# Kernel tuning notes

Hardware: AMD Instinct MI355X
Metric: run time of the kernel (lower is better)

The kernel has to match this reference:

```python
import jax, jax.numpy as jnp
import numpy as np

DIM = 1024
HEADS = 16
HD = DIM // HEADS
EPS = 1e-5


def setup_inputs() -> dict:
    key = jax.random.key(0)
    ks = jax.random.split(key, 7)
    s = 0.02
    return {
        "x": jax.random.normal(ks[0], (2, 2048, DIM), dtype=jnp.float32),
        "w_qkv": jax.random.normal(ks[1], (DIM, 3 * DIM), dtype=jnp.float32) * s,
        "b_qkv": jnp.zeros((3 * DIM,), dtype=jnp.float32),
        "g_q": jnp.ones((HD,), dtype=jnp.float32),
        "be_q": jnp.zeros((HD,), dtype=jnp.float32),
        "g_k": jnp.ones((HD,), dtype=jnp.float32),
        "be_k": jnp.zeros((HD,), dtype=jnp.float32),
        "w_proj": jax.random.normal(ks[2], (DIM, DIM), dtype=jnp.float32) * s,
        "b_proj": jnp.zeros((DIM,), dtype=jnp.float32),
    }


def _ln(x, g, b):
    mu = jnp.mean(x, axis=-1, keepdims=True)
    var = jnp.var(x, axis=-1, keepdims=True)
    return (x - mu) * jax.lax.rsqrt(var + EPS) * g + b


def reference(x, w_qkv, b_qkv, g_q, be_q, g_k, be_k, w_proj, b_proj):
    B, N, C = x.shape
    qkv = x @ w_qkv + b_qkv                      # [B,N,3C]
    qkv = qkv.reshape(B, N, 3, HEADS, HD).transpose(2, 0, 3, 1, 4)  # [3,B,H,N,hd]
    q, k, v = qkv[0], qkv[1], qkv[2]
    q = _ln(q, g_q, be_q) * (HD ** -0.5)
    k = _ln(k, g_k, be_k)
    attn = jax.nn.softmax(jnp.einsum("bhqd,bhkd->bhqk", q, k), axis=-1)
    out = jnp.einsum("bhqk,bhkd->bhqd", attn, v)  # [B,H,N,hd]
    out = out.transpose(0, 2, 1, 3).reshape(B, N, C)
    return out @ w_proj + b_proj
```

## Files before the change

### kernel.cpp

```cpp
#include <hip/hip_runtime.h>
#include <hip/hip_bf16.h>


typedef short bf16x8 __attribute__((ext_vector_type(8)));
typedef float f32x4  __attribute__((ext_vector_type(4)));

__device__ __forceinline__ short f2bf(float f) {
  union { float f; unsigned u; } c; c.f = f;
  unsigned r = c.u + 0x7fffu + ((c.u >> 16) & 1u);
  return (short)(r >> 16);
}

__device__ __forceinline__ unsigned pk2(float a, float b) {
  __hip_bfloat162 h = __float22bfloat162_rn(make_float2(a, b));
  unsigned u;
  __builtin_memcpy(&u, &h, 4);
  return u;
}

__device__ __forceinline__ void gld16(const void* g, void* l) {
  __builtin_amdgcn_global_load_lds(
      (const __attribute__((address_space(1))) unsigned int*)(unsigned long long)g,
      (__attribute__((address_space(3))) unsigned int*)(unsigned int)(unsigned long long)l,
      16, 0, 0);
}

__global__ void k_cvt(const float* __restrict__ in, short* __restrict__ out, int n) {
  int i = (blockIdx.x * blockDim.x + threadIdx.x) * 4;
  if (i < n) {
    float4 f = *(const float4*)(in + i);
    uint2 u;
    u.x = pk2(f.x, f.y);
    u.y = pk2(f.z, f.w);
    *(uint2*)(out + i) = u;
  }
}

__global__ void k_transpose(const float* __restrict__ in, short* __restrict__ out,
                            int R, int C) {
  __shared__ float t[32][33];
  const int tx = threadIdx.x, ty = threadIdx.y;
  const int c0 = blockIdx.x * 32, r0 = blockIdx.y * 32;
#pragma unroll
  for (int i = 0; i < 4; i++)
    t[ty * 4 + i][tx] = in[(size_t)(r0 + ty * 4 + i) * C + c0 + tx];
  __syncthreads();
#pragma unroll
  for (int i = 0; i < 4; i++)
    out[(size_t)(c0 + ty * 4 + i) * R + r0 + tx] = f2bf(t[tx][ty * 4 + i]);
}

__device__ __forceinline__ void mm_loop(const short* __restrict__ A,
                                        const short* __restrict__ B,
                                        int K, int mBase, int nBase,
                                        short* As, short* Bs, f32x4 acc[4][4]) {
  const int tid = threadIdx.x;
  const int w = tid >> 6, lane = tid & 63;
  const int wr = w >> 1, wc = w & 1;
  const int lhi = lane >> 4, llo = lane & 15;
  const int rin = lane >> 3;
  const int kin = (lane & 7) * 8;

  const f32x4 fz = {0.f, 0.f, 0.f, 0.f};
#pragma unroll
  for (int mi = 0; mi < 4; mi++)
#pragma unroll
    for (int ni = 0; ni < 4; ni++) acc[mi][ni] = fz;

  const int nkt = K >> 6;

  const short* pA[4];
  const short* pB[4];
#pragma unroll
  for (int i = 0; i < 4; i++) {
    const int row = (w * 4 + i) * 8 + rin;
    pA[i] = A + (size_t)(mBase + row) * K + kin;
    pB[i] = B + (size_t)(nBase + row) * K + kin;
  }

#define MMSTAGE(buf)                                                           \
  {                                                                            \
    _Pragma("unroll")                                                          \
    for (int i = 0; i < 4; i++) {                                              \
      const int c = w * 4 + i;                                                 \
      gld16(pA[i], As + (buf) * 8192 + c * 512);                               \
      gld16(pB[i], Bs + (buf) * 8192 + c * 512);                               \
      pA[i] += 64;                                                             \
      pB[i] += 64;                                                             \
    }                                                                          \
  }

  MMSTAGE(0);
  __syncthreads();
  int cur = 0;

  for (int kb = 0; kb < nkt; kb++) {
    if (kb + 1 < nkt) MMSTAGE(cur ^ 1);
    const short* Ac = As + cur * 8192;
    const short* Bc = Bs + cur * 8192;
#pragma unroll
    for (int kk = 0; kk < 2; kk++) {
      bf16x8 a[4], b[4];
#pragma unroll
      for (int mi = 0; mi < 4; mi++)
        a[mi] = *(const bf16x8*)(Ac + (wr * 64 + mi * 16 + llo) * 64 + kk * 32 + lhi * 8);
#pragma unroll
      for (int ni = 0; ni < 4; ni++)
        b[ni] = *(const bf16x8*)(Bc + (wc * 64 + ni * 16 + llo) * 64 + kk * 32 + lhi * 8);
#pragma unroll
      for (int mi = 0; mi < 4; mi++)
#pragma unroll
        for (int ni = 0; ni < 4; ni++)
          acc[mi][ni] = __builtin_amdgcn_mfma_f32_16x16x32_bf16(a[mi], b[ni], acc[mi][ni], 0, 0, 0);
    }
    __syncthreads();
    cur ^= 1;
  }
#undef MMSTAGE
}

__global__ __launch_bounds__(256) void k_gemm_qkv(
    const short* __restrict__ A, const short* __restrict__ B,
    const float* __restrict__ bqkv,
    const float* __restrict__ g_q, const float* __restrict__ be_q,
    const float* __restrict__ g_k, const float* __restrict__ be_k,
    short* __restrict__ Qg, short* __restrict__ Kg, short* __restrict__ Vtg) {
  __shared__ short As[2 * 8192];
  __shared__ short Bs[2 * 8192];
  f32x4 acc[4][4];
  const int mBase = blockIdx.x * 128, nBase = blockIdx.y * 128;
  mm_loop(A, B, 1024, mBase, nBase, As, Bs, acc);

  const int tid = threadIdx.x;
  const int w = tid >> 6, lane = tid & 63;
  const int wr = w >> 1, wc = w & 1;
  const int lhi = lane >> 4, llo = lane & 15;

  const int cg0 = nBase + wc * 64;
  const int t = cg0 >> 10;
  const int h = (cg0 & 1023) >> 6;

  float bias[4], gg[4], bb[4];
#pragma unroll
  for (int ni = 0; ni < 4; ni++) {
    const int d = ni * 16 + llo;
    bias[ni] = bqkv[cg0 + d];
    if (t == 0)      { gg[ni] = g_q[d]; bb[ni] = be_q[d]; }
    else if (t == 1) { gg[ni] = g_k[d]; bb[ni] = be_k[d]; }
    else             { gg[ni] = 1.f;    bb[ni] = 0.f; }
  }

#pragma unroll
  for (int mi = 0; mi < 4; mi++) {
    float v[4][4];
#pragma unroll
    for (int ni = 0; ni < 4; ni++)
#pragma unroll
      for (int j = 0; j < 4; j++) v[ni][j] = acc[mi][ni][j] + bias[ni];

    if (t < 2) {
#pragma unroll
      for (int j = 0; j < 4; j++) {
        float s = 0.f, s2 = 0.f;
#pragma unroll
        for (int ni = 0; ni < 4; ni++) { s += v[ni][j]; s2 += v[ni][j] * v[ni][j]; }
#pragma unroll
        for (int msk = 1; msk < 16; msk <<= 1) {
          s  += __shfl_xor(s,  msk, 64);
          s2 += __shfl_xor(s2, msk, 64);
        }
        const float mu = s * 0.015625f;
        const float var = s2 * 0.015625f - mu * mu;
        const float rs = rsqrtf(var + 1e-5f);
#pragma unroll
        for (int ni = 0; ni < 4; ni++) {
          float y = (v[ni][j] - mu) * rs * gg[ni] + bb[ni];
          if (t == 0) y *= 0.125f;
          v[ni][j] = y;
        }
      }
    }
    const int rbase = mBase + wr * 64 + mi * 16 + lhi * 4;
#pragma unroll
    for (int j = 0; j < 4; j++) {
      const int r = rbase + j;
      const int b_ = r >> 11;
      const int n = r & 2047;
      const int bh = b_ * 16 + h;
#pragma unroll
      for (int np = 0; np < 2; np++) {
        const int d0 = np * 32 + llo;
        const unsigned u = pk2(v[np * 2][j], v[np * 2 + 1][j]);
        const short lo = (short)(u & 0xffffu);
        const short hi = (short)(u >> 16);
        if (t == 0) {
          Qg[((size_t)bh * 2048 + n) * 64 + d0]      = lo;
          Qg[((size_t)bh * 2048 + n) * 64 + d0 + 16] = hi;
        } else if (t == 1) {
          Kg[((size_t)bh * 2048 + n) * 64 + d0]      = lo;
          Kg[((size_t)bh * 2048 + n) * 64 + d0 + 16] = hi;
        } else {
          Vtg[((size_t)bh * 64 + d0) * 2048 + n]        = lo;
          Vtg[((size_t)bh * 64 + d0 + 16) * 2048 + n]   = hi;
        }
      }
    }
  }
}

__global__ __launch_bounds__(256) void k_attn(const short* __restrict__ Qg,
                                              const short* __restrict__ Kg,
                                              const short* __restrict__ Vtg,
                                              short* __restrict__ aout) {
  __shared__ short KV[2][8192];
  __shared__ short Ps[4][1024];
  const int tid = threadIdx.x;
  const int w = tid >> 6, lane = tid & 63;
  const int lhi = lane >> 4, llo = lane & 15;
  const int rin = lane >> 3;
  const int tg = (lane & 7) ^ rin;
  const int bh = blockIdx.y;
  const int qrow0 = blockIdx.x * 64 + w * 16;

  const short* Qrow = Qg + ((size_t)bh * 2048 + qrow0 + llo) * 64;
  const bf16x8 qa0 = *(const bf16x8*)(Qrow + lhi * 8);
  const bf16x8 qa1 = *(const bf16x8*)(Qrow + 32 + lhi * 8);

  bf16x8 onesb;
#pragma unroll
  for (int e = 0; e < 8; e++) onesb[e] = (short)0x3F80;

  const f32x4 fz = {0.f, 0.f, 0.f, 0.f};
  f32x4 o[4];
#pragma unroll
  for (int dg = 0; dg < 4; dg++) o[dg] = fz;
  f32x4 lsum = fz;

  short* Pw = Ps[w];
  const size_t kbase = (size_t)bh * 2048;
  const size_t vbase = (size_t)bh * 64;

  const short* gp[4];
#pragma unroll
  for (int i = 0; i < 4; i++) {
    const int cc = w * 4 + i;
    gp[i] = (cc < 8)
        ? (Kg  + (kbase + (size_t)(cc * 8 + rin)) * 64 + tg * 8)
        : (Vtg + (vbase + (size_t)((cc - 8) * 8 + rin)) * 2048 + tg * 8);
  }
  const int gstride = (w < 2) ? 4096 : 64;

#define STAGE(buf)                                                             \
  {                                                                            \
    _Pragma("unroll")                                                          \
    for (int i = 0; i < 4; i++) {                                              \
      gld16(gp[i], &KV[buf][(w * 4 + i) * 512]);                               \
      gp[i] += gstride;                                                        \
    }                                                                          \
  }

  STAGE(0);
  __syncthreads();
  int cur = 0;

  for (int kt = 0; kt < 32; kt++) {
    if (kt < 31) STAGE(cur ^ 1);

    const short* Kc = KV[cur];
    const short* Vc = KV[cur] + 4096;

    f32x4 s[4];
    __builtin_amdgcn_s_setprio(1);
#pragma unroll
    for (int krg = 0; krg < 4; krg++) {
      const int rk = krg * 16 + llo;
      const int sw = rk & 7;
      const bf16x8 kb0 = *(const bf16x8*)(Kc + rk * 64 + ((lhi ^ sw)) * 8);
      const bf16x8 kb1 = *(const bf16x8*)(Kc + rk * 64 + (((4 + lhi) ^ sw)) * 8);
      f32x4 z = fz;
      z = __builtin_amdgcn_mfma_f32_16x16x32_bf16(kb0, qa0, z, 0, 0, 0);
      z = __builtin_amdgcn_mfma_f32_16x16x32_bf16(kb1, qa1, z, 0, 0, 0);
      s[krg] = z;
    }
    __builtin_amdgcn_s_setprio(0);

#pragma unroll
    for (int krg = 0; krg < 4; krg++) {
      const float p0 = __expf(s[krg][0]);
      const float p1 = __expf(s[krg][1]);
      const float p2 = __expf(s[krg][2]);
      const float p3 = __expf(s[krg][3]);
      uint2 u;
      u.x = pk2(p0, p1);
      u.y = pk2(p2, p3);
      char* pb = (char*)Pw + llo * 128 +
                 (((krg * 2 + (lhi >> 1)) ^ (llo & 7)) << 4) + ((lhi & 1) << 3);
      *(uint2*)pb = u;
    }

    const int swp = llo & 7;
    const bf16x8 pa0 = *(const bf16x8*)(Pw + llo * 64 + ((lhi ^ swp)) * 8);
    const bf16x8 pa1 = *(const bf16x8*)(Pw + llo * 64 + (((4 + lhi) ^ swp)) * 8);

    __builtin_amdgcn_s_setprio(1);
    lsum = __builtin_amdgcn_mfma_f32_16x16x32_bf16(pa0, onesb, lsum, 0, 0, 0);
    lsum = __builtin_amdgcn_mfma_f32_16x16x32_bf16(pa1, onesb, lsum, 0, 0, 0);

#pragma unroll
    for (int dg = 0; dg < 4; dg++) {
      const int rv = dg * 16 + llo;
      const int swv = rv & 7;
      const bf16x8 vb0 = *(const bf16x8*)(Vc + rv * 64 + ((lhi ^ swv)) * 8);
      const bf16x8 vb1 = *(const bf16x8*)(Vc + rv * 64 + (((4 + lhi) ^ swv)) * 8);
      o[dg] = __builtin_amdgcn_mfma_f32_16x16x32_bf16(pa0, vb0, o[dg], 0, 0, 0);
      o[dg] = __builtin_amdgcn_mfma_f32_16x16x32_bf16(pa1, vb1, o[dg], 0, 0, 0);
    }
    __builtin_amdgcn_s_setprio(0);
    __syncthreads();
    cur ^= 1;
  }
#undef STAGE

  const int b_ = bh >> 4, h = bh & 15;
#pragma unroll
  for (int j = 0; j < 4; j++) {
    const float inv = 1.f / lsum[j];
    const int n = qrow0 + lhi * 4 + j;
    short* arow = aout + ((size_t)(b_ * 2048 + n)) * 1024 + h * 64 + llo;
#pragma unroll
    for (int dp = 0; dp < 2; dp++) {
      const unsigned u = pk2(o[dp * 2][j] * inv, o[dp * 2 + 1][j] * inv);
      arow[dp * 32]      = (short)(u & 0xffffu);
      arow[dp * 32 + 16] = (short)(u >> 16);
    }
  }
}

__global__ __launch_bounds__(256) void k_gemm_proj(const short* __restrict__ A,
                                                   const short* __restrict__ B,
                                                   const float* __restrict__ bias,
                                                   float* __restrict__ C) {
  __shared__ short As[2 * 8192];
  __shared__ short Bs[2 * 8192];
  f32x4 acc[4][4];
  const int mBase = blockIdx.x * 128, nBase = blockIdx.y * 128;
  mm_loop(A, B, 1024, mBase, nBase, As, Bs, acc);

  const int tid = threadIdx.x;
  const int w = tid >> 6, lane = tid & 63;
  const int wr = w >> 1, wc = w & 1;
  const int lhi = lane >> 4, llo = lane & 15;
#pragma unroll
  for (int mi = 0; mi < 4; mi++)
#pragma unroll
    for (int ni = 0; ni < 4; ni++) {
      const int col = nBase + wc * 64 + ni * 16 + llo;
      const float bv = bias[col];
#pragma unroll
      for (int j = 0; j < 4; j++) {
        const int row = mBase + wr * 64 + mi * 16 + lhi * 4 + j;
        C[(size_t)row * 1024 + col] = acc[mi][ni][j] + bv;
      }
    }
}

extern "C" void kernel_launch(void* const* d_in, const int* in_sizes, int n_in,
                              void* d_out, int out_size, void* d_ws, size_t ws_size,
                              hipStream_t stream) {
  const float* x      = (const float*)d_in[0];
  const float* w_qkv  = (const float*)d_in[1];
  const float* b_qkv  = (const float*)d_in[2];
  const float* g_q    = (const float*)d_in[3];
  const float* be_q   = (const float*)d_in[4];
  const float* g_k    = (const float*)d_in[5];
  const float* be_k   = (const float*)d_in[6];
  const float* w_proj = (const float*)d_in[7];
  const float* b_proj = (const float*)d_in[8];
  float* out = (float*)d_out;

  char* ws = (char*)d_ws;
  short* xb     = (short*)(ws);
  short* wqkvT  = (short*)(ws + ((size_t)8  << 20));
  short* wprojT = (short*)(ws + ((size_t)14 << 20));
  short* Qg     = (short*)(ws + ((size_t)16 << 20));
  short* Kg     = (short*)(ws + ((size_t)24 << 20));
  short* Vtg    = (short*)(ws + ((size_t)32 << 20));
  short* aout   = (short*)(ws + ((size_t)40 << 20));

  k_cvt<<<4096, 256, 0, stream>>>(x, xb, 4096 * 1024);
  k_transpose<<<dim3(3072 / 32, 1024 / 32), dim3(32, 8), 0, stream>>>(w_qkv, wqkvT, 1024, 3072);
  k_transpose<<<dim3(1024 / 32, 1024 / 32), dim3(32, 8), 0, stream>>>(w_proj, wprojT, 1024, 1024);
  k_gemm_qkv<<<dim3(32, 24), 256, 0, stream>>>(xb, wqkvT, b_qkv, g_q, be_q, g_k, be_k, Qg, Kg, Vtg);
  k_attn<<<dim3(32, 32), 256, 0, stream>>>(Qg, Kg, Vtg, aout);
  k_gemm_proj<<<dim3(32, 8), 256, 0, stream>>>(aout, wprojT, b_proj, out);
}
```

Measured before the change: 218.0 us.

## Use partial vmcnt waits with raw barriers and remap attention blocks per XCD

In both the GEMM main loop and the attention loop, the full __syncthreads (which drains all outstanding loads) is replaced by an explicit s_waitcnt vmcnt(N) plus s_barrier. This lets the prefetch of the next stage stay in flight while the current stage is consumed, so load latency overlaps with compute. The attention launch also becomes a 1D grid whose block index is remapped so consecutive blocks landing on the same XCD share the same head, which should improve K/V reuse in L2. The risk is that the hand-set vmcnt counts must exactly match the number of issued global_load_lds ops, or LDS data could be read before it arrives.

Result: no change. 219.3 us (+0.6%).

```diff
diff --git a/kernel.cpp b/kernel.cpp
--- a/kernel.cpp
+++ b/kernel.cpp
@@ -91,11 +91,17 @@
   }
 
   MMSTAGE(0);
-  __syncthreads();
   int cur = 0;
 
   for (int kb = 0; kb < nkt; kb++) {
-    if (kb + 1 < nkt) MMSTAGE(cur ^ 1);
+    if (kb + 1 < nkt) {
+      MMSTAGE(cur ^ 1);
+      asm volatile("s_waitcnt vmcnt(8)" ::: "memory");
+    } else {
+      asm volatile("s_waitcnt vmcnt(0)" ::: "memory");
+    }
+    __builtin_amdgcn_s_barrier();
+    __builtin_amdgcn_sched_barrier(0);
     const short* Ac = As + cur * 8192;
     const short* Bc = Bs + cur * 8192;
 #pragma unroll
@@ -113,7 +119,7 @@
         for (int ni = 0; ni < 4; ni++)
           acc[mi][ni] = __builtin_amdgcn_mfma_f32_16x16x32_bf16(a[mi], b[ni], acc[mi][ni], 0, 0, 0);
     }
-    __syncthreads();
+    __builtin_amdgcn_s_barrier();
     cur ^= 1;
   }
 #undef MMSTAGE
@@ -219,8 +225,11 @@
   const int lhi = lane >> 4, llo = lane & 15;
   const int rin = lane >> 3;
   const int tg = (lane & 7) ^ rin;
-  const int bh = blockIdx.y;
-  const int qrow0 = blockIdx.x * 64 + w * 16;
+
+  const int b = blockIdx.x;
+  const int w2 = (b & 7) * 128 + (b >> 3);
+  const int bh = w2 >> 5;
+  const int qrow0 = (w2 & 31) * 64 + w * 16;
 
   const short* Qrow = Qg + ((size_t)bh * 2048 + qrow0 + llo) * 64;
   const bf16x8 qa0 = *(const bf16x8*)(Qrow + lhi * 8);
@@ -260,11 +269,17 @@
   }
 
   STAGE(0);
-  __syncthreads();
   int cur = 0;
 
   for (int kt = 0; kt < 32; kt++) {
-    if (kt < 31) STAGE(cur ^ 1);
+    if (kt < 31) {
+      STAGE(cur ^ 1);
+      asm volatile("s_waitcnt vmcnt(4)" ::: "memory");
+    } else {
+      asm volatile("s_waitcnt vmcnt(0)" ::: "memory");
+    }
+    __builtin_amdgcn_s_barrier();
+    __builtin_amdgcn_sched_barrier(0);
 
     const short* Kc = KV[cur];
     const short* Vc = KV[cur] + 4096;
@@ -316,7 +331,7 @@
       o[dg] = __builtin_amdgcn_mfma_f32_16x16x32_bf16(pa1, vb1, o[dg], 0, 0, 0);
     }
     __builtin_amdgcn_s_setprio(0);
-    __syncthreads();
+    __builtin_amdgcn_s_barrier();
     cur ^= 1;
   }
 #undef STAGE
@@ -391,6 +406,6 @@
   k_transpose<<<dim3(3072 / 32, 1024 / 32), dim3(32, 8), 0, stream>>>(w_qkv, wqkvT, 1024, 3072);
   k_transpose<<<dim3(1024 / 32, 1024 / 32), dim3(32, 8), 0, stream>>>(w_proj, wprojT, 1024, 1024);
   k_gemm_qkv<<<dim3(32, 24), 256, 0, stream>>>(xb, wqkvT, b_qkv, g_q, be_q, g_k, be_k, Qg, Kg, Vtg);
-  k_attn<<<dim3(32, 32), 256, 0, stream>>>(Qg, Kg, Vtg, aout);
+  k_attn<<<1024, 256, 0, stream>>>(Qg, Kg, Vtg, aout);
   k_gemm_proj<<<dim3(32, 8), 256, 0, stream>>>(aout, wprojT, b_proj, out);
 }
```
